# Kernel optimization log

Measured on AMD Instinct MI355X. Metric: run time of the kernel, lower is better.

Reference implementation:

```python
import jax, jax.numpy as jnp
import numpy as np

B, N, CIN, FOUT = 4, 512, 64, 64
EPS = 1e-5
NEG_SLOPE = 0.2


def setup_inputs() -> dict:
    key = jax.random.key(0)
    ks = jax.random.split(key, 10)
    s = lambda k, shape: (jax.random.normal(k, shape, dtype=jnp.float32) * 0.05)
    return {
        "x": jax.random.normal(ks[0], (B, N, CIN), dtype=jnp.float32),
        "adj": jax.random.uniform(ks[1], (N, N), dtype=jnp.float32),
        "W_w": s(ks[2], (FOUT, CIN)), "W_b": s(ks[3], (FOUT,)),
        "U_w": s(ks[4], (FOUT, FOUT)), "U_b": s(ks[5], (FOUT,)),
        "V_w": s(ks[6], (FOUT, FOUT)), "V_b": s(ks[7], (FOUT,)),
        "att_w": s(ks[8], (1, 2 * FOUT)), "att_b": s(ks[9], (1,)),
        "ln_g": jnp.ones((FOUT,), jnp.float32),
        "ln_b": jnp.zeros((FOUT,), jnp.float32),
    }


def reference(x, adj, W_w, W_b, U_w, U_b, V_w, V_b, att_w, att_b, ln_g, ln_b):
    # h = W(x): (B, N, F)
    h = x @ W_w.T + W_b
    Fd = h.shape[-1]
    # attention(cat[h_i, h_j]) == (h_i @ a_i) + (h_j @ a_j) + b  -> avoid (B,N,N,2F)
    a_i, a_j = att_w[0, :Fd], att_w[0, Fd:]
    logits = (h @ a_i)[:, :, None] + (h @ a_j)[:, None, :] + att_b[0]  # (B,N,N)
    logits = jnp.where(logits > 0, logits, NEG_SLOPE * logits)  # LeakyReLU(0.2)
    attn = jax.nn.softmax(logits, axis=-1)  # softmax over j; dropout is identity in eval
    # gate = sigmoid(U(h_i) + V(h_j)); U/V applied once per node then broadcast
    Uh = h @ U_w.T + U_b  # (B,N,F)
    Vh = h @ V_w.T + V_b  # (B,N,F)
    gate = jax.nn.sigmoid(Uh[:, :, None, :] + Vh[:, None, :, :])  # (B,N,N,F)
    node_features = gate * attn[..., None] * h[:, None, :, :]  # (B,N,N,F)
    # aggr[b,i,f] = sum_{j,k} nf[b,i,j,f] * adj[j,k]
    aggr = jnp.einsum('bijf,jk->bif', node_features, adj)
    # LayerNorm over last dim
    mu = jnp.mean(aggr, axis=-1, keepdims=True)
    var = jnp.var(aggr, axis=-1, keepdims=True)
    out = (aggr - mu) / jnp.sqrt(var + EPS) * ln_g + ln_b
    return out
```

## Files before the change

kernel.cpp:

```cpp
#include <hip/hip_runtime.h>

#define NB 4
#define NN 512
#define NF 64
#define NEG_SLOPE 0.2f
#define LN_EPS 1e-5f
#define WP 66

__device__ __forceinline__ float wave_sum(float v){
  #pragma unroll
  for (int d = 32; d; d >>= 1) v += __shfl_xor(v, d, 64);
  return v;
}
__device__ __forceinline__ float wave_max(float v){
  #pragma unroll
  for (int d = 32; d; d >>= 1) v = fmaxf(v, __shfl_xor(v, d, 64));
  return v;
}
__device__ __forceinline__ unsigned int rnd_bf_hi(float f){
  union { float f; unsigned int i; } v; v.f = f;
  return (v.i + 0x7fffu + ((v.i >> 16) & 1u)) & 0xffff0000u;
}


extern "C" __global__ __launch_bounds__(256, 2)
void k_setup(const float* __restrict__ x, const float* __restrict__ adj,
             const float* __restrict__ Ww, const float* __restrict__ Wb,
             const float* __restrict__ Uw, const float* __restrict__ Ub,
             const float* __restrict__ Vw, const float* __restrict__ Vb,
             const float* __restrict__ attw,
             float* __restrict__ ws)
{
  float* r            = ws;
  unsigned int* evh   = (unsigned int*)(ws + NN);
  float* eU           = ws + NN + NB*NN*NF;
  float* li           = eU + NB*NN*NF;
  float* lj           = li + NB*NN;

  __shared__ float s_w[3*64*WP];
  __shared__ float s_x[4][NF];
  __shared__ float s_h[4][NF];
  __shared__ float s_red[4];

  const int tid  = threadIdx.x;
  const int w    = tid >> 6;
  const int lane = tid & 63;
  const int g    = blockIdx.x;
  const int row  = g*4 + w;

  {
    const float4* srcs[3] = { (const float4*)Ww, (const float4*)Uw, (const float4*)Vw };
    #pragma unroll
    for (int m = 0; m < 3; m++){
      const float4* src = srcs[m];
      #pragma unroll
      for (int k = 0; k < 4; k++){
        int idx4 = tid + k*256;
        float4 v = src[idx4];
        int e = idx4 * 4;
        int f = e >> 6, c = e & 63;
        float* dst = &s_w[m*64*WP + f*WP + c];
        dst[0] = v.x; dst[1] = v.y; dst[2] = v.z; dst[3] = v.w;
      }
    }
  }
  s_x[w][lane] = x[row*NF + lane];
  __syncthreads();

  float hv = Wb[lane];
  {
    const float* wr = &s_w[0*64*WP + lane*WP];
    #pragma unroll
    for (int c = 0; c < NF; c += 2){
      float2 xb = *(const float2*)&s_x[w][c];
      float2 wv = *(const float2*)&wr[c];
      hv = fmaf(xb.x, wv.x, hv);
      hv = fmaf(xb.y, wv.y, hv);
    }
  }
  s_h[w][lane] = hv;
  __syncthreads();

  float uh = Ub[lane];
  float vh = Vb[lane];
  {
    const float* ur = &s_w[1*64*WP + lane*WP];
    const float* vr = &s_w[2*64*WP + lane*WP];
    #pragma unroll
    for (int c = 0; c < NF; c += 2){
      float2 hb = *(const float2*)&s_h[w][c];
      float2 uv = *(const float2*)&ur[c];
      float2 vv = *(const float2*)&vr[c];
      uh = fmaf(hb.x, uv.x, uh); uh = fmaf(hb.y, uv.y, uh);
      vh = fmaf(hb.x, vv.x, vh); vh = fmaf(hb.y, vv.y, vh);
    }
  }

  float ev = __expf(-vh);
  float eu = __expf(-uh);
  evh[row*NF + lane] = rnd_bf_hi(hv) | (rnd_bf_hi(ev) >> 16);
  eU[row*NF + lane] = eu;

  float pi = wave_sum(hv * attw[lane]);
  float pj = wave_sum(hv * attw[NF + lane]);
  if (lane == 0){ li[row] = pi; lj[row] = pj; }

  {
    const float2* a2 = (const float2*)(adj + g*NN);
    float2 a = a2[tid];
    float s = wave_sum(a.x + a.y);
    if (lane == 0) s_red[w] = s;
    __syncthreads();
    if (tid == 0) r[g] = s_red[0] + s_red[1] + s_red[2] + s_red[3];
  }
}

extern "C" __global__ __launch_bounds__(256)
void k_main(const float* __restrict__ attb_p,
            const float* __restrict__ lng,
            const float* __restrict__ lnb,
            const float* __restrict__ ws,
            float* __restrict__ out)
{
  const float* r          = ws;
  const unsigned int* evh = (const unsigned int*)(ws + NN);
  const float* eU         = ws + NN + NB*NN*NF;
  const float* li         = eU + NB*NN*NF;
  const float* lj         = li + NB*NN;

  __shared__ float s_c[NN][4];
  __shared__ float s_part[4][4][NF];

  const int tid  = threadIdx.x;
  const int w    = tid >> 6;
  const int lane = tid & 63;
  const int b    = blockIdx.x >> 7;
  const int i0   = (blockIdx.x & 127) * 4;
  const int i    = i0 + w;

  const float attb = attb_p[0];
  const float li_s = li[b*NN + i];

  float lv[8];
  float m = -1e30f;
  #pragma unroll
  for (int t = 0; t < 8; t++){
    int j = lane + 64*t;
    float l = li_s + lj[b*NN + j] + attb;
    l = (l > 0.f) ? l : NEG_SLOPE*l;
    lv[t] = l;
    m = fmaxf(m, l);
  }
  m = wave_max(m);
  float S = 0.f;
  #pragma unroll
  for (int t = 0; t < 8; t++){ lv[t] = __expf(lv[t] - m); S += lv[t]; }
  S = wave_sum(S);
  float inv = __builtin_amdgcn_rcpf(S);
  #pragma unroll
  for (int t = 0; t < 8; t++){
    int j = lane + 64*t;
    s_c[j][w] = lv[t]*inv*r[j];
  }

  const float eu0 = eU[(b*NN + i0 + 0)*NF + lane];
  const float eu1 = eU[(b*NN + i0 + 1)*NF + lane];
  const float eu2 = eU[(b*NN + i0 + 2)*NF + lane];
  const float eu3 = eU[(b*NN + i0 + 3)*NF + lane];

  __syncthreads();

  const unsigned int* evhb = evh + (size_t)(b*NN)*NF;
  float a0 = 0.f, a1 = 0.f, a2 = 0.f, a3 = 0.f;
  const int j0 = w*128;
  #pragma unroll 8
  for (int jj = 0; jj < 128; jj++){
    int j = j0 + jj;
    unsigned int u = evhb[j*NF + lane];
    union { unsigned int i; float f; } hh, ee;
    hh.i = u & 0xffff0000u;
    ee.i = u << 16;
    float4 c4 = *(const float4*)&s_c[j][0];
    float q0 = fmaf(eu0, ee.f, 1.0f);
    float q1 = fmaf(eu1, ee.f, 1.0f);
    float q2 = fmaf(eu2, ee.f, 1.0f);
    float q3 = fmaf(eu3, ee.f, 1.0f);
    a0 = fmaf(c4.x, hh.f * __builtin_amdgcn_rcpf(q0), a0);
    a1 = fmaf(c4.y, hh.f * __builtin_amdgcn_rcpf(q1), a1);
    a2 = fmaf(c4.z, hh.f * __builtin_amdgcn_rcpf(q2), a2);
    a3 = fmaf(c4.w, hh.f * __builtin_amdgcn_rcpf(q3), a3);
  }

  s_part[w][0][lane] = a0;
  s_part[w][1][lane] = a1;
  s_part[w][2][lane] = a2;
  s_part[w][3][lane] = a3;
  __syncthreads();

  float acc = s_part[0][w][lane] + s_part[1][w][lane]
            + s_part[2][w][lane] + s_part[3][w][lane];

  float s1 = wave_sum(acc);
  float s2 = wave_sum(acc*acc);
  float mu  = s1 * (1.f/NF);
  float var = s2 * (1.f/NF) - mu*mu;
  float rs  = __builtin_amdgcn_rsqf(var + LN_EPS);
  float o = (acc - mu)*rs*lng[lane] + lnb[lane];
  out[(b*NN + i)*NF + lane] = o;
}

extern "C" void kernel_launch(void* const* d_in, const int* in_sizes, int n_in,
                              void* d_out, int out_size, void* d_ws, size_t ws_size,
                              hipStream_t stream)
{
  const float* x    = (const float*)d_in[0];
  const float* adj  = (const float*)d_in[1];
  const float* Ww   = (const float*)d_in[2];
  const float* Wb   = (const float*)d_in[3];
  const float* Uw   = (const float*)d_in[4];
  const float* Ub   = (const float*)d_in[5];
  const float* Vw   = (const float*)d_in[6];
  const float* Vb   = (const float*)d_in[7];
  const float* attw = (const float*)d_in[8];
  const float* attb = (const float*)d_in[9];
  const float* lng  = (const float*)d_in[10];
  const float* lnb  = (const float*)d_in[11];
  float* ws = (float*)d_ws;
  float* outp = (float*)d_out;

  hipLaunchKernelGGL(k_setup, dim3(NN), dim3(256), 0, stream,
                     x, adj, Ww, Wb, Uw, Ub, Vw, Vb, attw, ws);
  hipLaunchKernelGGL(k_main, dim3(NB*NN/4), dim3(256), 0, stream,
                     attb, lng, lnb, ws, outp);
}
```

Baseline: 94.14 us.

## Fuse setup and main kernels into one cooperative kernel with grid sync

Merges the setup kernel (projections, gate exponentials, attention logits, adj row sums) and the aggregation/LayerNorm kernel into a single cooperative launch of 512 blocks. The two phases are separated by a grid-wide barrier, and their shared memory is overlaid through a union. This removes the second kernel launch and the gap between launches. In exchange it adds the cost of a grid barrier, needs all 512 blocks to be co-resident, and drops the occupancy hint on the setup phase.

```diff
diff --git a/kernel.cpp b/kernel.cpp
--- a/kernel.cpp
+++ b/kernel.cpp
@@ -1,4 +1,7 @@
 #include <hip/hip_runtime.h>
+#include <hip/hip_cooperative_groups.h>
+
+namespace cg = cooperative_groups;
 
 #define NB 4
 #define NN 512
@@ -23,13 +26,14 @@
 }
 
 
-extern "C" __global__ __launch_bounds__(256, 2)
-void k_setup(const float* __restrict__ x, const float* __restrict__ adj,
+extern "C" __global__ __launch_bounds__(256)
+void k_fused(const float* __restrict__ x, const float* __restrict__ adj,
              const float* __restrict__ Ww, const float* __restrict__ Wb,
              const float* __restrict__ Uw, const float* __restrict__ Ub,
              const float* __restrict__ Vw, const float* __restrict__ Vb,
-             const float* __restrict__ attw,
-             float* __restrict__ ws)
+             const float* __restrict__ attw, const float* __restrict__ attb_p,
+             const float* __restrict__ lng, const float* __restrict__ lnb,
+             float* __restrict__ ws, float* __restrict__ out)
 {
   float* r            = ws;
   unsigned int* evh   = (unsigned int*)(ws + NN);
@@ -37,18 +41,19 @@
   float* li           = eU + NB*NN*NF;
   float* lj           = li + NB*NN;
 
-  __shared__ float s_w[3*64*WP];
-  __shared__ float s_x[4][NF];
-  __shared__ float s_h[4][NF];
-  __shared__ float s_red[4];
+  __shared__ union SM {
+    struct { float w[3*64*WP]; float xx[4][NF]; float h[4][NF]; float red[4]; } a;
+    struct { float c[NN][4]; float part[4][4][NF]; } b;
+  } sm;
 
   const int tid  = threadIdx.x;
   const int w    = tid >> 6;
   const int lane = tid & 63;
   const int g    = blockIdx.x;
-  const int row  = g*4 + w;
 
   {
+    const int row = g*4 + w;
+
     const float4* srcs[3] = { (const float4*)Ww, (const float4*)Uw, (const float4*)Vw };
     #pragma unroll
     for (int m = 0; m < 3; m++){
@@ -59,154 +64,138 @@
         float4 v = src[idx4];
         int e = idx4 * 4;
         int f = e >> 6, c = e & 63;
-        float* dst = &s_w[m*64*WP + f*WP + c];
+        float* dst = &sm.a.w[m*64*WP + f*WP + c];
         dst[0] = v.x; dst[1] = v.y; dst[2] = v.z; dst[3] = v.w;
       }
     }
+    sm.a.xx[w][lane] = x[row*NF + lane];
+    __syncthreads();
+
+    float hv = Wb[lane];
+    {
+      const float* wr = &sm.a.w[0*64*WP + lane*WP];
+      #pragma unroll
+      for (int c = 0; c < NF; c += 2){
+        float2 xb = *(const float2*)&sm.a.xx[w][c];
+        float2 wv = *(const float2*)&wr[c];
+        hv = fmaf(xb.x, wv.x, hv);
+        hv = fmaf(xb.y, wv.y, hv);
+      }
+    }
+    sm.a.h[w][lane] = hv;
+    __syncthreads();
+
+    float uh = Ub[lane];
+    float vh = Vb[lane];
+    {
+      const float* ur = &sm.a.w[1*64*WP + lane*WP];
+      const float* vr = &sm.a.w[2*64*WP + lane*WP];
+      #pragma unroll
+      for (int c = 0; c < NF; c += 2){
+        float2 hb = *(const float2*)&sm.a.h[w][c];
+        float2 uv = *(const float2*)&ur[c];
+        float2 vv = *(const float2*)&vr[c];
+        uh = fmaf(hb.x, uv.x, uh); uh = fmaf(hb.y, uv.y, uh);
+        vh = fmaf(hb.x, vv.x, vh); vh = fmaf(hb.y, vv.y, vh);
+      }
+    }
+
+    float ev = __expf(-vh);
+    float eu = __expf(-uh);
+    evh[row*NF + lane] = rnd_bf_hi(hv) | (rnd_bf_hi(ev) >> 16);
+    eU[row*NF + lane] = eu;
+
+    float pi = wave_sum(hv * attw[lane]);
+    float pj = wave_sum(hv * attw[NF + lane]);
+    if (lane == 0){ li[row] = pi; lj[row] = pj; }
+
+    {
+      const float2* a2 = (const float2*)(adj + g*NN);
+      float2 a = a2[tid];
+      float s = wave_sum(a.x + a.y);
+      if (lane == 0) sm.a.red[w] = s;
+      __syncthreads();
+      if (tid == 0) r[g] = sm.a.red[0] + sm.a.red[1] + sm.a.red[2] + sm.a.red[3];
+    }
   }
-  s_x[w][lane] = x[row*NF + lane];
-  __syncthreads();
-
-  float hv = Wb[lane];
+
+  cg::this_grid().sync();
+
   {
-    const float* wr = &s_w[0*64*WP + lane*WP];
-    #pragma unroll
-    for (int c = 0; c < NF; c += 2){
-      float2 xb = *(const float2*)&s_x[w][c];
-      float2 wv = *(const float2*)&wr[c];
-      hv = fmaf(xb.x, wv.x, hv);
-      hv = fmaf(xb.y, wv.y, hv);
-    }
+    const int b  = g >> 7;
+    const int i0 = (g & 127) * 4;
+    const int i  = i0 + w;
+
+    const float attb = attb_p[0];
+    const float li_s = li[b*NN + i];
+
+    float lv[8];
+    float m = -1e30f;
+    #pragma unroll
+    for (int t = 0; t < 8; t++){
+      int j = lane + 64*t;
+      float l = li_s + lj[b*NN + j] + attb;
+      l = (l > 0.f) ? l : NEG_SLOPE*l;
+      lv[t] = l;
+      m = fmaxf(m, l);
+    }
+    m = wave_max(m);
+    float S = 0.f;
+    #pragma unroll
+    for (int t = 0; t < 8; t++){ lv[t] = __expf(lv[t] - m); S += lv[t]; }
+    S = wave_sum(S);
+    float inv = __builtin_amdgcn_rcpf(S);
+    #pragma unroll
+    for (int t = 0; t < 8; t++){
+      int j = lane + 64*t;
+      sm.b.c[j][w] = lv[t]*inv*r[j];
+    }
+
+    const float eu0 = eU[(b*NN + i0 + 0)*NF + lane];
+    const float eu1 = eU[(b*NN + i0 + 1)*NF + lane];
+    const float eu2 = eU[(b*NN + i0 + 2)*NF + lane];
+    const float eu3 = eU[(b*NN + i0 + 3)*NF + lane];
+
+    __syncthreads();
+
+    const unsigned int* evhb = evh + (size_t)(b*NN)*NF;
+    float a0 = 0.f, a1 = 0.f, a2 = 0.f, a3 = 0.f;
+    const int j0 = w*128;
+    #pragma unroll 8
+    for (int jj = 0; jj < 128; jj++){
+      int j = j0 + jj;
+      unsigned int u = evhb[j*NF + lane];
+      union { unsigned int i; float f; } hh, ee;
+      hh.i = u & 0xffff0000u;
+      ee.i = u << 16;
+      float4 c4 = *(const float4*)&sm.b.c[j][0];
+      float q0 = fmaf(eu0, ee.f, 1.0f);
+      float q1 = fmaf(eu1, ee.f, 1.0f);
+      float q2 = fmaf(eu2, ee.f, 1.0f);
+      float q3 = fmaf(eu3, ee.f, 1.0f);
+      a0 = fmaf(c4.x, hh.f * __builtin_amdgcn_rcpf(q0), a0);
+      a1 = fmaf(c4.y, hh.f * __builtin_amdgcn_rcpf(q1), a1);
+      a2 = fmaf(c4.z, hh.f * __builtin_amdgcn_rcpf(q2), a2);
+      a3 = fmaf(c4.w, hh.f * __builtin_amdgcn_rcpf(q3), a3);
+    }
+
+    sm.b.part[w][0][lane] = a0;
+    sm.b.part[w][1][lane] = a1;
+    sm.b.part[w][2][lane] = a2;
+    sm.b.part[w][3][lane] = a3;
+    __syncthreads();
+
+    float acc = sm.b.part[0][w][lane] + sm.b.part[1][w][lane]
+              + sm.b.part[2][w][lane] + sm.b.part[3][w][lane];
+
+    float s1 = wave_sum(acc);
+    float s2 = wave_sum(acc*acc);
+    float mu  = s1 * (1.f/NF);
+    float var = s2 * (1.f/NF) - mu*mu;
+    float rs  = __builtin_amdgcn_rsqf(var + LN_EPS);
+    float o = (acc - mu)*rs*lng[lane] + lnb[lane];
+    out[(b*NN + i)*NF + lane] = o;
   }
-  s_h[w][lane] = hv;
-  __syncthreads();
-
-  float uh = Ub[lane];
-  float vh = Vb[lane];
-  {
-    const float* ur = &s_w[1*64*WP + lane*WP];
-    const float* vr = &s_w[2*64*WP + lane*WP];
-    #pragma unroll
-    for (int c = 0; c < NF; c += 2){
-      float2 hb = *(const float2*)&s_h[w][c];
-      float2 uv = *(const float2*)&ur[c];
-      float2 vv = *(const float2*)&vr[c];
-      uh = fmaf(hb.x, uv.x, uh); uh = fmaf(hb.y, uv.y, uh);
-      vh = fmaf(hb.x, vv.x, vh); vh = fmaf(hb.y, vv.y, vh);
-    }
-  }
-
-  float ev = __expf(-vh);
-  float eu = __expf(-uh);
-  evh[row*NF + lane] = rnd_bf_hi(hv) | (rnd_bf_hi(ev) >> 16);
-  eU[row*NF + lane] = eu;
-
-  float pi = wave_sum(hv * attw[lane]);
-  float pj = wave_sum(hv * attw[NF + lane]);
-  if (lane == 0){ li[row] = pi; lj[row] = pj; }
-
-  {
-    const float2* a2 = (const float2*)(adj + g*NN);
-    float2 a = a2[tid];
-    float s = wave_sum(a.x + a.y);
-    if (lane == 0) s_red[w] = s;
-    __syncthreads();
-    if (tid == 0) r[g] = s_red[0] + s_red[1] + s_red[2] + s_red[3];
-  }
-}
-
-extern "C" __global__ __launch_bounds__(256)
-void k_main(const float* __restrict__ attb_p,
-            const float* __restrict__ lng,
-            const float* __restrict__ lnb,
-            const float* __restrict__ ws,
-            float* __restrict__ out)
-{
-  const float* r          = ws;
-  const unsigned int* evh = (const unsigned int*)(ws + NN);
-  const float* eU         = ws + NN + NB*NN*NF;
-  const float* li         = eU + NB*NN*NF;
-  const float* lj         = li + NB*NN;
-
-  __shared__ float s_c[NN][4];
-  __shared__ float s_part[4][4][NF];
-
-  const int tid  = threadIdx.x;
-  const int w    = tid >> 6;
-  const int lane = tid & 63;
-  const int b    = blockIdx.x >> 7;
-  const int i0   = (blockIdx.x & 127) * 4;
-  const int i    = i0 + w;
-
-  const float attb = attb_p[0];
-  const float li_s = li[b*NN + i];
-
-  float lv[8];
-  float m = -1e30f;
-  #pragma unroll
-  for (int t = 0; t < 8; t++){
-    int j = lane + 64*t;
-    float l = li_s + lj[b*NN + j] + attb;
-    l = (l > 0.f) ? l : NEG_SLOPE*l;
-    lv[t] = l;
-    m = fmaxf(m, l);
-  }
-  m = wave_max(m);
-  float S = 0.f;
-  #pragma unroll
-  for (int t = 0; t < 8; t++){ lv[t] = __expf(lv[t] - m); S += lv[t]; }
-  S = wave_sum(S);
-  float inv = __builtin_amdgcn_rcpf(S);
-  #pragma unroll
-  for (int t = 0; t < 8; t++){
-    int j = lane + 64*t;
-    s_c[j][w] = lv[t]*inv*r[j];
-  }
-
-  const float eu0 = eU[(b*NN + i0 + 0)*NF + lane];
-  const float eu1 = eU[(b*NN + i0 + 1)*NF + lane];
-  const float eu2 = eU[(b*NN + i0 + 2)*NF + lane];
-  const float eu3 = eU[(b*NN + i0 + 3)*NF + lane];
-
-  __syncthreads();
-
-  const unsigned int* evhb = evh + (size_t)(b*NN)*NF;
-  float a0 = 0.f, a1 = 0.f, a2 = 0.f, a3 = 0.f;
-  const int j0 = w*128;
-  #pragma unroll 8
-  for (int jj = 0; jj < 128; jj++){
-    int j = j0 + jj;
-    unsigned int u = evhb[j*NF + lane];
-    union { unsigned int i; float f; } hh, ee;
-    hh.i = u & 0xffff0000u;
-    ee.i = u << 16;
-    float4 c4 = *(const float4*)&s_c[j][0];
-    float q0 = fmaf(eu0, ee.f, 1.0f);
-    float q1 = fmaf(eu1, ee.f, 1.0f);
-    float q2 = fmaf(eu2, ee.f, 1.0f);
-    float q3 = fmaf(eu3, ee.f, 1.0f);
-    a0 = fmaf(c4.x, hh.f * __builtin_amdgcn_rcpf(q0), a0);
-    a1 = fmaf(c4.y, hh.f * __builtin_amdgcn_rcpf(q1), a1);
-    a2 = fmaf(c4.z, hh.f * __builtin_amdgcn_rcpf(q2), a2);
-    a3 = fmaf(c4.w, hh.f * __builtin_amdgcn_rcpf(q3), a3);
-  }
-
-  s_part[w][0][lane] = a0;
-  s_part[w][1][lane] = a1;
-  s_part[w][2][lane] = a2;
-  s_part[w][3][lane] = a3;
-  __syncthreads();
-
-  float acc = s_part[0][w][lane] + s_part[1][w][lane]
-            + s_part[2][w][lane] + s_part[3][w][lane];
-
-  float s1 = wave_sum(acc);
-  float s2 = wave_sum(acc*acc);
-  float mu  = s1 * (1.f/NF);
-  float var = s2 * (1.f/NF) - mu*mu;
-  float rs  = __builtin_amdgcn_rsqf(var + LN_EPS);
-  float o = (acc - mu)*rs*lng[lane] + lnb[lane];
-  out[(b*NN + i)*NF + lane] = o;
 }
 
 extern "C" void kernel_launch(void* const* d_in, const int* in_sizes, int n_in,
@@ -225,11 +214,11 @@
   const float* attb = (const float*)d_in[9];
   const float* lng  = (const float*)d_in[10];
   const float* lnb  = (const float*)d_in[11];
-  float* ws = (float*)d_ws;
+  float* ws   = (float*)d_ws;
   float* outp = (float*)d_out;
 
-  hipLaunchKernelGGL(k_setup, dim3(NN), dim3(256), 0, stream,
-                     x, adj, Ww, Wb, Uw, Ub, Vw, Vb, attw, ws);
-  hipLaunchKernelGGL(k_main, dim3(NB*NN/4), dim3(256), 0, stream,
-                     attb, lng, lnb, ws, outp);
-}
+  void* args[14] = { &x, &adj, &Ww, &Wb, &Uw, &Ub, &Vw, &Vb,
+                     &attw, &attb, &lng, &lnb, &ws, &outp };
+  hipLaunchCooperativeKernel((const void*)k_fused, dim3(NN), dim3(256),
+                             args, 0, stream);
+}
```

Measured after the change: 164.1 us. +74.3%, slower.
